# Kernel tuning notes

Measured on AMD Instinct MI355X. Metric: run time of the kernel, lower is better.

Reference implementation:

```python
import jax, jax.numpy as jnp
import numpy as np

NUM_HEADS = 8
GN_GROUPS = 8
GN_EPS = 1e-5


def setup_inputs() -> dict:
    key = jax.random.key(0)
    k1, k2, k3 = jax.random.split(key, 3)
    B, C, H, W = 8, 512, 32, 32
    x = jax.random.normal(k1, (B, C, H, W), dtype=jnp.float32)
    w_qkv = jax.random.normal(k2, (3 * C, C), dtype=jnp.float32) * 0.02
    w_proj = jax.random.normal(k3, (C, C), dtype=jnp.float32) * 0.02
    gamma = jnp.ones((C,), dtype=jnp.float32)
    beta = jnp.zeros((C,), dtype=jnp.float32)
    return {"x": x, "w_qkv": w_qkv, "w_proj": w_proj, "gamma": gamma, "beta": beta}


def reference(x, w_qkv, w_proj, gamma, beta):
    B, C, H, W = x.shape
    nh = NUM_HEADS
    hd = C // nh
    N = H * W
    scale = jnp.asarray(hd, x.dtype) ** -0.5

    xf = x.reshape(B, C, N)                                  # [B,C,N]
    # 1x1 conv (no bias) == channel matmul
    qkv = jnp.einsum('oc,bcn->bon', w_qkv, xf)               # [B,3C,N]
    qkv = qkv.reshape(B, 3, nh, hd, N)
    q, k, v = qkv[:, 0], qkv[:, 1], qkv[:, 2]                # [B,h,d,N]

    attn = jnp.einsum('bhdn,bhdm->bhnm', q, k) * scale       # [B,h,N,N]
    attn = jax.nn.softmax(attn, axis=-1)
    out = jnp.einsum('bhnm,bhdm->bhdn', attn, v)             # [B,h,d,N]
    out = out.reshape(B, C, N)

    out = jnp.einsum('oc,bcn->bon', w_proj, out).reshape(B, C, H, W)

    # GroupNorm(8, C)
    g = GN_GROUPS
    og = out.reshape(B, g, C // g, H, W)
    mean = og.mean(axis=(2, 3, 4), keepdims=True)
    var = og.var(axis=(2, 3, 4), keepdims=True)
    normed = ((og - mean) * jax.lax.rsqrt(var + GN_EPS)).reshape(B, C, H, W)
    normed = normed * gamma[None, :, None, None] + beta[None, :, None, None]

    return normed + x
```

## Files before the change

### kernel.cpp

```cpp
#include <hip/hip_runtime.h>

#define B_DIM 8
#define GN_EPS 1e-5f

typedef short s16x8 __attribute__((ext_vector_type(8)));
typedef float f32x4 __attribute__((ext_vector_type(4)));
typedef unsigned int u32x2 __attribute__((ext_vector_type(2)));
typedef s16x8 s16x8_a __attribute__((may_alias));
typedef u32x2 u32x2_a __attribute__((may_alias));

__device__ inline unsigned short f2bf(float f) {
    unsigned u = __builtin_bit_cast(unsigned, f);
    u += 0x7fffu + ((u >> 16) & 1u);
    return (unsigned short)(u >> 16);
}

__device__ inline unsigned cvtpk(float lo, float hi) {
    unsigned r;
    asm("v_cvt_pk_bf16_f32 %0, %1, %2" : "=v"(r) : "v"(lo), "v"(hi));
    return r;
}

__device__ inline f32x4 mfma16(s16x8 a, s16x8 b, f32x4 c) {
    return __builtin_amdgcn_mfma_f32_16x16x32_bf16(a, b, c, 0, 0, 0);
}

__device__ inline void gload16(const unsigned short* g, unsigned short* l) {
    __builtin_amdgcn_global_load_lds(
        (const __attribute__((address_space(1))) unsigned int*)g,
        (__attribute__((address_space(3))) unsigned int*)l, 16, 0, 0);
}

#define WAIT_VM4() asm volatile("s_waitcnt vmcnt(4)" : : : "memory")
#define WAIT_VM0() asm volatile("s_waitcnt vmcnt(0)" : : : "memory")
#define BAR() __builtin_amdgcn_s_barrier()
#define SFENCE() __builtin_amdgcn_sched_barrier(0)

#define SWZ(r, c) ((r)*64 + ((c) ^ (((r)&7) << 3)))

__global__ __launch_bounds__(256)
void prep_kernel(const float* __restrict__ x, const float* __restrict__ wq,
                 const float* __restrict__ wp, unsigned short* __restrict__ xt,
                 unsigned short* __restrict__ wqb, unsigned short* __restrict__ wpb) {
    const int bid = blockIdx.x, t = threadIdx.x;
    __shared__ float ts[64][65];
    if (bid < 1024) {
        const int ntile = bid & 15, ctile = (bid >> 4) & 7, b = bid >> 7;
        const float* xp = x + ((size_t)b * 512 + ctile * 64) * 1024 + ntile * 64;
        #pragma unroll
        for (int i = 0; i < 16; ++i) {
            int f = i * 256 + t; int c = f >> 6, n = f & 63;
            ts[n][c] = xp[(size_t)c * 1024 + n];
        }
        __syncthreads();
        unsigned short* xo = xt + ((size_t)b * 1024 + ntile * 64) * 512 + ctile * 64;
        #pragma unroll
        for (int i = 0; i < 8; ++i) {
            int f = i * 512 + t * 2; int n = f >> 6, c = f & 63;
            unsigned lo = f2bf(ts[n][c]);
            unsigned hi = f2bf(ts[n][c + 1]);
            *(unsigned int*)&xo[(size_t)n * 512 + c] = lo | (hi << 16);
        }
    } else {
        const float4* src; unsigned short* dst; int idx;
        if (bid < 1792) { idx = (bid - 1024) * 256 + t; src = (const float4*)wq; dst = wqb; }
        else            { idx = (bid - 1792) * 256 + t; src = (const float4*)wp; dst = wpb; }
        float4 v = src[idx];
        ushort4 pk;
        pk.x = f2bf(v.x); pk.y = f2bf(v.y); pk.z = f2bf(v.z); pk.w = f2bf(v.w);
        *(ushort4*)&dst[(size_t)idx * 4] = pk;
    }
}

template<int O_DIM, int MODE>
__global__ __launch_bounds__(256)
void mm_kernel(const unsigned short* __restrict__ Wb,
               const unsigned short* __restrict__ Xt,
               unsigned short* __restrict__ proj_bf,
               unsigned short* __restrict__ qt,
               unsigned short* __restrict__ kt,
               unsigned short* __restrict__ vt,
               float* __restrict__ partial) {
    constexpr int OT = O_DIM / 128;
    const int bi = blockIdx.x;
    const int nt = bi & 7;
    const int rest = bi >> 3;
    const int ot = rest % OT;
    const int b  = rest / OT;

    const int t = threadIdx.x;
    const int w = t >> 6, lid = t & 63, lr = lid & 15, g4 = lid >> 4;
    const int wr = w >> 1, wc = w & 1;

    __shared__ unsigned short lds[24576];

    const unsigned short* wsrc = Wb + ((size_t)(ot * 128 + w * 32 + (lid >> 2))) * 512 + (lid & 3) * 8;
    const unsigned short* xsrc = Xt + ((size_t)b * 1024 + nt * 128 + w * 32 + (lid >> 2)) * 512 + (lid & 3) * 8;
    const int woff0 = (w * 32) * 32;
    const int woff1 = (w * 32 + 16) * 32;

    const f32x4 Z4 = {0.f, 0.f, 0.f, 0.f};
    f32x4 acc[4][4];
    #pragma unroll
    for (int i = 0; i < 4; ++i)
        #pragma unroll
        for (int j = 0; j < 4; ++j) acc[i][j] = Z4;

    #pragma unroll
    for (int p = 0; p < 2; ++p) {
        unsigned short* nb = lds + p * 8192;
        const int k0 = p * 32;
        gload16(wsrc + k0, nb + woff0);
        gload16(wsrc + k0 + 16 * 512, nb + woff1);
        gload16(xsrc + k0, nb + 4096 + woff0);
        gload16(xsrc + k0 + 16 * 512, nb + 4096 + woff1);
    }
    WAIT_VM4(); BAR(); SFENCE();

    #pragma unroll 1
    for (int it = 0; it < 16; ++it) {
        unsigned short* buf = lds + (it % 3) * 8192;
        if (it <= 13) {
            const int k2 = (it + 2) * 32;
            unsigned short* nb = lds + ((it + 2) % 3) * 8192;
            gload16(wsrc + k2, nb + woff0);
            gload16(wsrc + k2 + 16 * 512, nb + woff1);
            gload16(xsrc + k2, nb + 4096 + woff0);
            gload16(xsrc + k2 + 16 * 512, nb + 4096 + woff1);
        }
        s16x8 av[4], bv[4];
        #pragma unroll
        for (int mi = 0; mi < 4; ++mi)
            av[mi] = *(const s16x8*)&buf[(wr * 64 + mi * 16 + lr) * 32 + g4 * 8];
        #pragma unroll
        for (int nj = 0; nj < 4; ++nj)
            bv[nj] = *(const s16x8*)&buf[4096 + (wc * 64 + nj * 16 + lr) * 32 + g4 * 8];
        #pragma unroll
        for (int mi = 0; mi < 4; ++mi)
            #pragma unroll
            for (int nj = 0; nj < 4; ++nj)
                acc[mi][nj] = mfma16(av[mi], bv[nj], acc[mi][nj]);
        if (it <= 13)      { WAIT_VM4(); BAR(); SFENCE(); }
        else if (it == 14) { WAIT_VM0(); BAR(); SFENCE(); }
    }

    if (MODE == 2) {
        float s1 = 0.f, s2 = 0.f;
        #pragma unroll
        for (int mi = 0; mi < 4; ++mi)
            #pragma unroll
            for (int nj = 0; nj < 4; ++nj)
                #pragma unroll
                for (int r = 0; r < 4; ++r) {
                    float v = acc[mi][nj][r];
                    s1 += v;
                    s2 += v * v;
                }
        #pragma unroll
        for (int off = 1; off <= 32; off <<= 1) {
            s1 += __shfl_xor(s1, off);
            s2 += __shfl_xor(s2, off);
        }
        if (lid == 0) {
            float2* pp = (float2*)partial + ((size_t)(b * 8 + ot * 2 + wr) * 16)
                         + nt * 2 + wc;
            *pp = make_float2(s1, s2);
        }
    }

    __syncthreads();
    unsigned short* T = lds + w * 4352;
    const int obase = ot * 128 + wr * 64;
    const int j16 = lid & 15, r4 = lid >> 4;
    const size_t n0w = (size_t)nt * 128 + wc * 64;

    if (MODE == 1) {
        const int s = obase >> 9;
        const int h = (obase >> 6) & 7;
        const float scl = (s == 0) ? 0.18033688f : 1.0f;
        #pragma unroll
        for (int mi = 0; mi < 4; ++mi)
            #pragma unroll
            for (int nj = 0; nj < 4; ++nj)
                #pragma unroll
                for (int r = 0; r < 4; ++r) {
                    int ol = mi * 16 + g4 * 4 + r, nl = nj * 16 + lr;
                    unsigned short v = f2bf(acc[mi][nj][r] * scl);
                    T[(s < 2) ? (nl * 68 + ol) : (ol * 68 + nl)] = v;
                }
        unsigned short* obuf = ((s == 0) ? qt : (s == 1) ? kt : vt)
                               + ((size_t)(b * 8 + h) * 1024 + n0w) * 64;
        #pragma unroll
        for (int p = 0; p < 16; ++p) {
            int rw = p * 4 + r4;
            u32x2 v = *(const u32x2_a*)&T[rw * 68 + 4 * j16];
            *(u32x2_a*)(obuf + rw * 64 + 4 * j16) = v;
        }
    } else {
        #pragma unroll
        for (int mi = 0; mi < 4; ++mi)
            #pragma unroll
            for (int nj = 0; nj < 4; ++nj)
                #pragma unroll
                for (int r = 0; r < 4; ++r)
                    T[(mi * 16 + g4 * 4 + r) * 68 + nj * 16 + lr] = f2bf(acc[mi][nj][r]);
        #pragma unroll
        for (int p = 0; p < 16; ++p) {
            int rw = p * 4 + r4;
            u32x2 v = *(const u32x2_a*)&T[rw * 68 + 4 * j16];
            *(u32x2_a*)(proj_bf + ((size_t)(b * 512 + obase + rw)) * 1024
                        + nt * 128 + wc * 64 + 4 * j16) = v;
        }
    }
}

__global__ __launch_bounds__(256)
void attn_kernel(const unsigned short* __restrict__ qt,
                 const unsigned short* __restrict__ kt,
                 const unsigned short* __restrict__ vt,
                 unsigned short* __restrict__ aout) {
    const int bi = blockIdx.x;
    const int h = bi & 7;
    const int qtile = (bi >> 3) & 7;
    const int b = bi >> 6;

    const int t = threadIdx.x;
    const int w = t >> 6, lid = t & 63, lr = lid & 15, g4 = lid >> 4;
    const int rr = lid >> 3, cc = lid & 7;
    const int csw = (cc ^ rr) << 3;

    __shared__ unsigned short lds[32768];
    unsigned short* Ps = lds + 24576;

    const unsigned short* qbh = qt + ((size_t)b * 8 + h) * 65536;
    const unsigned short* kbh = kt + ((size_t)b * 8 + h) * 65536;
    const unsigned short* vbh = vt + ((size_t)b * 8 + h) * 65536;

    s16x8 qa[2][2];
    #pragma unroll
    for (int mi = 0; mi < 2; ++mi)
        #pragma unroll
        for (int ks = 0; ks < 2; ++ks)
            qa[mi][ks] = *(const s16x8*)(qbh +
                (size_t)(qtile * 128 + w * 32 + mi * 16 + lr) * 64 + ks * 32 + g4 * 8);

    #pragma unroll
    for (int p = 0; p < 2; ++p) {
        unsigned short* Kd = lds + p * 4096;
        unsigned short* Vd = lds + 12288 + p * 4096;
        const int m = p * 64;
        #pragma unroll
        for (int i2 = 0; i2 < 2; ++i2) {
            gload16(kbh + (size_t)(m + w * 16 + i2 * 8 + rr) * 64 + csw,
                    Kd + (w * 16 + i2 * 8) * 64);
            gload16(vbh + (size_t)(m + w * 16 + i2 * 8 + rr) * 64 + csw,
                    Vd + (w * 16 + i2 * 8) * 64);
        }
    }
    WAIT_VM4(); BAR(); SFENCE();

    const f32x4 Z4 = {0.f, 0.f, 0.f, 0.f};
    f32x4 acc_o[2][4];
    float l_run[2] = {0.f, 0.f};
    #pragma unroll
    for (int mi = 0; mi < 2; ++mi)
        #pragma unroll
        for (int di = 0; di < 4; ++di) acc_o[mi][di] = Z4;

    #pragma unroll 1
    for (int it = 0; it < 16; ++it) {
        unsigned short* Kc = lds + (it % 3) * 4096;
        unsigned short* Vc = lds + 12288 + (it % 3) * 4096;

        if (it <= 13) {
            const int m2 = (it + 2) * 64;
            unsigned short* Kd = lds + ((it + 2) % 3) * 4096;
            unsigned short* Vd = lds + 12288 + ((it + 2) % 3) * 4096;
            #pragma unroll
            for (int i2 = 0; i2 < 2; ++i2) {
                gload16(kbh + (size_t)(m2 + w * 16 + i2 * 8 + rr) * 64 + csw,
                        Kd + (w * 16 + i2 * 8) * 64);
                gload16(vbh + (size_t)(m2 + w * 16 + i2 * 8 + rr) * 64 + csw,
                        Vd + (w * 16 + i2 * 8) * 64);
            }
        }

        f32x4 sc[2][4];
        #pragma unroll
        for (int mi = 0; mi < 2; ++mi)
            #pragma unroll
            for (int mj = 0; mj < 4; ++mj) sc[mi][mj] = Z4;
        #pragma unroll
        for (int ks = 0; ks < 2; ++ks) {
            s16x8 kb[4];
            #pragma unroll
            for (int mj = 0; mj < 4; ++mj)
                kb[mj] = *(const s16x8*)&Kc[SWZ(mj * 16 + lr, ks * 32 + g4 * 8)];
            #pragma unroll
            for (int mi = 0; mi < 2; ++mi)
                #pragma unroll
                for (int mj = 0; mj < 4; ++mj)
                    sc[mi][mj] = mfma16(kb[mj], qa[mi][ks], sc[mi][mj]);
        }

        #pragma unroll
        for (int mi = 0; mi < 2; ++mi) {
            #pragma unroll
            for (int mj = 0; mj < 4; ++mj) {
                float p0 = __builtin_amdgcn_exp2f(sc[mi][mj][0]);
                float p1 = __builtin_amdgcn_exp2f(sc[mi][mj][1]);
                float p2 = __builtin_amdgcn_exp2f(sc[mi][mj][2]);
                float p3 = __builtin_amdgcn_exp2f(sc[mi][mj][3]);
                l_run[mi] += (p0 + p1) + (p2 + p3);
                u32x2 pk;
                pk.x = cvtpk(p0, p1);
                pk.y = cvtpk(p2, p3);
                *(u32x2_a*)&Ps[SWZ(w * 32 + mi * 16 + lr, mj * 16 + g4 * 4)] = pk;
            }
        }

        s16x8 vb[2][4];
        #pragma unroll
        for (int ks = 0; ks < 2; ++ks)
            #pragma unroll
            for (int di = 0; di < 4; ++di)
                vb[ks][di] = *(const s16x8*)&Vc[SWZ(di * 16 + lr, ks * 32 + g4 * 8)];

        #pragma unroll
        for (int ks = 0; ks < 2; ++ks) {
            s16x8 pa[2];
            #pragma unroll
            for (int mi = 0; mi < 2; ++mi)
                pa[mi] = *(const s16x8_a*)&Ps[SWZ(w * 32 + mi * 16 + lr, ks * 32 + g4 * 8)];
            #pragma unroll
            for (int mi = 0; mi < 2; ++mi)
                #pragma unroll
                for (int di = 0; di < 4; ++di)
                    acc_o[mi][di] = mfma16(pa[mi], vb[ks][di], acc_o[mi][di]);
        }
        if (it <= 13)      { WAIT_VM4(); BAR(); SFENCE(); }
        else if (it == 14) { WAIT_VM0(); BAR(); SFENCE(); }
    }

    #pragma unroll
    for (int mi = 0; mi < 2; ++mi) {
        float l = l_run[mi];
        l += __shfl_xor(l, 16);
        l += __shfl_xor(l, 32);
        l_run[mi] = 1.f / l;
    }
    #pragma unroll
    for (int mi = 0; mi < 2; ++mi) {
        float inv[4];
        #pragma unroll
        for (int r = 0; r < 4; ++r)
            inv[r] = __shfl(l_run[mi], g4 * 4 + r);
        #pragma unroll
        for (int di = 0; di < 4; ++di)
            #pragma unroll
            for (int r = 0; r < 4; ++r) {
                int n = qtile * 128 + w * 32 + mi * 16 + g4 * 4 + r;
                int c = h * 64 + di * 16 + lr;
                aout[((size_t)b * 1024 + n) * 512 + c] = f2bf(acc_o[mi][di][r] * inv[r]);
            }
    }
}

__global__ __launch_bounds__(256)
void gn_apply_kernel(const unsigned short* __restrict__ pb,
                     const float* __restrict__ partial, const float* __restrict__ x,
                     const float* __restrict__ gamma, const float* __restrict__ beta,
                     float* __restrict__ out) {
    const int qtr = blockIdx.x;
    const int g = blockIdx.y;
    const int b = blockIdx.z;
    const int t = threadIdx.x;
    const float2* pp = (const float2*)partial + (size_t)(b * 8 + g) * 16;
    float sum = 0.f, sq = 0.f;
    #pragma unroll
    for (int s = 0; s < 16; ++s) { sum += pp[s].x; sq += pp[s].y; }
    const float mean = sum * (1.f / 65536.f);
    const float var  = sq * (1.f / 65536.f) - mean * mean;
    const float rstd = rsqrtf(var + GN_EPS);
    #pragma unroll
    for (int j = 0; j < 2; ++j) {
        const int c = g * 64 + qtr * 4 + j * 2 + (t >> 7);
        const float gm = gamma[c] * rstd, bt = beta[c];
        const size_t base = ((size_t)b * 512 + c) * 1024 + (t & 127) * 8;
        s16x8 pv = *(const s16x8_a*)(pb + base);
        float4 xa = *(const float4*)(x + base);
        float4 xb = *(const float4*)(x + base + 4);
        float4 ra, rb;
        ra.x = (__builtin_bit_cast(float, ((unsigned)(unsigned short)pv[0]) << 16) - mean) * gm + bt + xa.x;
        ra.y = (__builtin_bit_cast(float, ((unsigned)(unsigned short)pv[1]) << 16) - mean) * gm + bt + xa.y;
        ra.z = (__builtin_bit_cast(float, ((unsigned)(unsigned short)pv[2]) << 16) - mean) * gm + bt + xa.z;
        ra.w = (__builtin_bit_cast(float, ((unsigned)(unsigned short)pv[3]) << 16) - mean) * gm + bt + xa.w;
        rb.x = (__builtin_bit_cast(float, ((unsigned)(unsigned short)pv[4]) << 16) - mean) * gm + bt + xb.x;
        rb.y = (__builtin_bit_cast(float, ((unsigned)(unsigned short)pv[5]) << 16) - mean) * gm + bt + xb.y;
        rb.z = (__builtin_bit_cast(float, ((unsigned)(unsigned short)pv[6]) << 16) - mean) * gm + bt + xb.z;
        rb.w = (__builtin_bit_cast(float, ((unsigned)(unsigned short)pv[7]) << 16) - mean) * gm + bt + xb.w;
        *(float4*)(out + base) = ra;
        *(float4*)(out + base + 4) = rb;
    }
}

extern "C" void kernel_launch(void* const* d_in, const int* in_sizes, int n_in,
                              void* d_out, int out_size, void* d_ws, size_t ws_size,
                              hipStream_t stream) {
    (void)in_sizes; (void)n_in; (void)out_size; (void)ws_size;
    const float* x      = (const float*)d_in[0];
    const float* w_qkv  = (const float*)d_in[1];
    const float* w_proj = (const float*)d_in[2];
    const float* gamma  = (const float*)d_in[3];
    const float* beta   = (const float*)d_in[4];
    float* out = (float*)d_out;

    unsigned short* qtb  = (unsigned short*)d_ws;
    unsigned short* ktb  = qtb  + 4194304;
    unsigned short* vtb  = ktb  + 4194304;
    unsigned short* aoutb= vtb  + 4194304;
    unsigned short* xtb  = aoutb+ 4194304;
    unsigned short* pbf  = xtb  + 4194304;
    unsigned short* wqb  = pbf  + 4194304;
    unsigned short* wpb  = wqb  + 786432;
    float* partial = (float*)(wpb + 262144);

    prep_kernel<<<2048, 256, 0, stream>>>(x, w_qkv, w_proj, xtb, wqb, wpb);
    mm_kernel<1536, 1><<<768, 256, 0, stream>>>(wqb, xtb, nullptr, qtb, ktb, vtb, nullptr);
    attn_kernel<<<512, 256, 0, stream>>>(qtb, ktb, vtb, aoutb);
    mm_kernel<512, 2><<<256, 256, 0, stream>>>(wpb, aoutb, pbf, nullptr, nullptr, nullptr, partial);
    gn_apply_kernel<<<dim3(16, 8, B_DIM), 256, 0, stream>>>(pbf, partial, x, gamma, beta, out);
}
```

Baseline: 76.20 us.

## Load K/V fragments directly from global memory instead of LDS pipeline

Removes the triple-buffered asynchronous global-to-LDS staging of K and V tiles in the attention kernel. Each wave now reads its MFMA operand fragments for K and V straight from global memory, which drops the per-iteration barriers and cuts LDS use to only the P buffer. The cost is that every wave fetches the same K/V data on its own, relying on cache for reuse, and it loses the prefetch overlap. The P scratch in LDS still uses the swizzled layout.

```diff
diff --git a/kernel.cpp b/kernel.cpp
--- a/kernel.cpp
+++ b/kernel.cpp
@@ -226,11 +226,8 @@
 
     const int t = threadIdx.x;
     const int w = t >> 6, lid = t & 63, lr = lid & 15, g4 = lid >> 4;
-    const int rr = lid >> 3, cc = lid & 7;
-    const int csw = (cc ^ rr) << 3;
-
-    __shared__ unsigned short lds[32768];
-    unsigned short* Ps = lds + 24576;
+
+    __shared__ unsigned short Ps[8192];
 
     const unsigned short* qbh = qt + ((size_t)b * 8 + h) * 65536;
     const unsigned short* kbh = kt + ((size_t)b * 8 + h) * 65536;
@@ -244,21 +241,6 @@
             qa[mi][ks] = *(const s16x8*)(qbh +
                 (size_t)(qtile * 128 + w * 32 + mi * 16 + lr) * 64 + ks * 32 + g4 * 8);
 
-    #pragma unroll
-    for (int p = 0; p < 2; ++p) {
-        unsigned short* Kd = lds + p * 4096;
-        unsigned short* Vd = lds + 12288 + p * 4096;
-        const int m = p * 64;
-        #pragma unroll
-        for (int i2 = 0; i2 < 2; ++i2) {
-            gload16(kbh + (size_t)(m + w * 16 + i2 * 8 + rr) * 64 + csw,
-                    Kd + (w * 16 + i2 * 8) * 64);
-            gload16(vbh + (size_t)(m + w * 16 + i2 * 8 + rr) * 64 + csw,
-                    Vd + (w * 16 + i2 * 8) * 64);
-        }
-    }
-    WAIT_VM4(); BAR(); SFENCE();
-
     const f32x4 Z4 = {0.f, 0.f, 0.f, 0.f};
     f32x4 acc_o[2][4];
     float l_run[2] = {0.f, 0.f};
@@ -269,21 +251,8 @@
 
     #pragma unroll 1
     for (int it = 0; it < 16; ++it) {
-        unsigned short* Kc = lds + (it % 3) * 4096;
-        unsigned short* Vc = lds + 12288 + (it % 3) * 4096;
-
-        if (it <= 13) {
-            const int m2 = (it + 2) * 64;
-            unsigned short* Kd = lds + ((it + 2) % 3) * 4096;
-            unsigned short* Vd = lds + 12288 + ((it + 2) % 3) * 4096;
-            #pragma unroll
-            for (int i2 = 0; i2 < 2; ++i2) {
-                gload16(kbh + (size_t)(m2 + w * 16 + i2 * 8 + rr) * 64 + csw,
-                        Kd + (w * 16 + i2 * 8) * 64);
-                gload16(vbh + (size_t)(m2 + w * 16 + i2 * 8 + rr) * 64 + csw,
-                        Vd + (w * 16 + i2 * 8) * 64);
-            }
-        }
+        const unsigned short* kc = kbh + it * 4096;
+        const unsigned short* vc = vbh + it * 4096;
 
         f32x4 sc[2][4];
         #pragma unroll
@@ -295,7 +264,7 @@
             s16x8 kb[4];
             #pragma unroll
             for (int mj = 0; mj < 4; ++mj)
-                kb[mj] = *(const s16x8*)&Kc[SWZ(mj * 16 + lr, ks * 32 + g4 * 8)];
+                kb[mj] = *(const s16x8_a*)(kc + (mj * 16 + lr) * 64 + ks * 32 + g4 * 8);
             #pragma unroll
             for (int mi = 0; mi < 2; ++mi)
                 #pragma unroll
@@ -324,7 +293,7 @@
         for (int ks = 0; ks < 2; ++ks)
             #pragma unroll
             for (int di = 0; di < 4; ++di)
-                vb[ks][di] = *(const s16x8*)&Vc[SWZ(di * 16 + lr, ks * 32 + g4 * 8)];
+                vb[ks][di] = *(const s16x8_a*)(vc + (di * 16 + lr) * 64 + ks * 32 + g4 * 8);
 
         #pragma unroll
         for (int ks = 0; ks < 2; ++ks) {
@@ -338,8 +307,6 @@
                 for (int di = 0; di < 4; ++di)
                     acc_o[mi][di] = mfma16(pa[mi], vb[ks][di], acc_o[mi][di]);
         }
-        if (it <= 13)      { WAIT_VM4(); BAR(); SFENCE(); }
-        else if (it == 14) { WAIT_VM0(); BAR(); SFENCE(); }
     }
 
     #pragma unroll
```

Result: slower. 111.0 us (+45.7%).
